# Kernel tuning notes

Hardware: AMD Instinct MI355X
Metric: run time of the kernel (lower is better)

Reference implementation:

```python
import jax, jax.numpy as jnp
import numpy as np

IN_FEATURES = 1024
OUT_FEATURES = 256
BATCH = 131072
EPS = 1e-4


def setup_inputs() -> dict:
    key = jax.random.key(0)
    kx, kw, kb = jax.random.split(key, 3)
    x = jax.random.normal(kx, (BATCH, IN_FEATURES), dtype=jnp.float32)
    # nn.Linear default init: U(-1/sqrt(in), 1/sqrt(in)) for both W and b
    bound = 1.0 / np.sqrt(IN_FEATURES)
    W = jax.random.uniform(kw, (OUT_FEATURES, IN_FEATURES), dtype=jnp.float32, minval=-bound, maxval=bound)
    b = jax.random.uniform(kb, (OUT_FEATURES,), dtype=jnp.float32, minval=-bound, maxval=bound)
    return {"x": x, "W": W, "b": b}


def reference(x, W, b):
    # L2-normalize each row (dim=1), matching x / (||x||_2 + 1e-4)
    norm = jnp.sqrt(jnp.sum(x * x, axis=1, keepdims=True))
    x_dir = x / (norm + EPS)
    # Linear: x_dir @ W^T + b, then ReLU
    h = jnp.einsum('bi,oi->bo', x_dir, W) + b
    return jax.nn.relu(h)
```

## Files before the change

kernel.cpp:

```cpp
#include <hip/hip_runtime.h>


#define IN_F   1024
#define OUT_F  256
#define BATCH  131072
#define BM     128
#define NKT    32
#define EPSV   1e-4f

typedef __attribute__((ext_vector_type(8))) __bf16 bf16x8;
typedef __attribute__((ext_vector_type(4))) __bf16 bf16x4;
typedef __attribute__((ext_vector_type(4))) float  f32x4;

__device__ __forceinline__ void gload_lds16(const void* g, void* lds) {
  __builtin_amdgcn_global_load_lds(
      (const __attribute__((address_space(1))) void*)g,
      (__attribute__((address_space(3))) void*)lds, 16, 0, 0);
}

#define VM_WAIT(N) do { asm volatile("s_waitcnt vmcnt(" #N ")" ::: "memory"); \
                        __builtin_amdgcn_sched_barrier(0); } while (0)

__global__ void wconv_kernel(const float* __restrict__ W, __bf16* __restrict__ Wb) {
  const int t = blockIdx.x * blockDim.x + threadIdx.x;
  const float4 v = reinterpret_cast<const float4*>(W)[t];
  bf16x4 h;
  h[0] = (__bf16)v.x; h[1] = (__bf16)v.y; h[2] = (__bf16)v.z; h[3] = (__bf16)v.w;
  reinterpret_cast<bf16x4*>(Wb)[t] = h;
}

__global__ __launch_bounds__(512, 2)
void ffl_kernel(const float* __restrict__ x, const __bf16* __restrict__ Wb,
                const float* __restrict__ bias, float* __restrict__ out) {
  __shared__ __align__(16) char smem[163840];
  char* const Ab[3] = {smem, smem + 32768, smem + 65536};
  char* const Bb[4] = {smem + 98304, smem + 114688, smem + 131072, smem + 147456};

  const int tid  = threadIdx.x;
  const int lane = tid & 63;
  const int wave = tid >> 6;
  const int wr   = wave >> 2;
  const int wc   = wave & 3;
  const int rm   = lane & 15;
  const int q    = lane >> 4;
  const size_t block_row = (size_t)blockIdx.x * BM;
  const int phg = blockIdx.x & 15;

  const float* aSrc[4]; int aDst[4];
  #pragma unroll
  for (int i = 0; i < 4; ++i) {
    const int c   = 4 * wave + i;
    const int row = 4 * c + (lane >> 4);
    const int s   = (lane & 15) ^ (row & 7);
    aSrc[i] = x + (block_row + row) * IN_F + s * 4;
    aDst[i] = c * 1024;
  }
  const __bf16* bSrc[2]; int bDst[2];
  #pragma unroll
  for (int i = 0; i < 2; ++i) {
    const int c    = 2 * wave + i;
    const int brow = 16 * c + (lane >> 2);
    const int bs   = (lane & 3) ^ ((brow >> 1) & 3);
    bSrc[i] = Wb + (size_t)brow * IN_F + bs * 8;
    bDst[i] = c * 1024;
  }

  f32x4 acc[4][4];
  #pragma unroll
  for (int m = 0; m < 4; ++m)
    #pragma unroll
    for (int n = 0; n < 4; ++n)
      acc[m][n] = (f32x4){0.f, 0.f, 0.f, 0.f};

  float ssq[4] = {0.f, 0.f, 0.f, 0.f};

  auto stageA = [&](int g) {
    const int pg = (g + phg) & 15;
    #pragma unroll
    for (int i = 0; i < 4; ++i)
      gload_lds16(aSrc[i] + pg * 64, Ab[g % 3] + aDst[i]);
  };
  auto stageB = [&](int kt) {
    const int pk = (kt + 2 * phg) & 31;
    #pragma unroll
    for (int i = 0; i < 2; ++i)
      gload_lds16(bSrc[i] + pk * 32, Bb[kt & 3] + bDst[i]);
  };

  stageA(0);
  stageB(0);
  stageA(1);
  stageB(1);
  stageB(2);
  VM_WAIT(8);
  __builtin_amdgcn_s_barrier();

  #pragma unroll
  for (int kt = 0; kt < NKT; ++kt) {
    if (kt + 3 < NKT) stageB(kt + 3);
    if ((kt & 1) == 0 && (kt / 2 + 2) < 16) stageA(kt / 2 + 2);

    const char* abuf = Ab[(kt >> 1) % 3];
    const char* bbuf = Bb[kt & 3];
    const int   gb   = (kt & 1) * 8 + 2 * q;

    bf16x8 aF[4];
    #pragma unroll
    for (int m = 0; m < 4; ++m) {
      const int ra = wr * 64 + m * 16 + rm;
      const char* ab = abuf + ra * 256;
      const int sw = ra & 7;
      const f32x4 lo = *reinterpret_cast<const f32x4*>(ab + ((gb)     ^ sw) * 16);
      const f32x4 hi = *reinterpret_cast<const f32x4*>(ab + ((gb + 1) ^ sw) * 16);
      ssq[m] += lo[0]*lo[0] + lo[1]*lo[1] + lo[2]*lo[2] + lo[3]*lo[3]
              + hi[0]*hi[0] + hi[1]*hi[1] + hi[2]*hi[2] + hi[3]*hi[3];
      bf16x8 a;
      a[0]=(__bf16)lo[0]; a[1]=(__bf16)lo[1]; a[2]=(__bf16)lo[2]; a[3]=(__bf16)lo[3];
      a[4]=(__bf16)hi[0]; a[5]=(__bf16)hi[1]; a[6]=(__bf16)hi[2]; a[7]=(__bf16)hi[3];
      aF[m] = a;
    }

    #pragma unroll
    for (int n = 0; n < 4; ++n) {
      const int rb = wc * 64 + n * 16 + rm;
      const bf16x8 bF = *reinterpret_cast<const bf16x8*>(
          bbuf + rb * 64 + (q ^ ((rb >> 1) & 3)) * 16);
      #pragma unroll
      for (int m = 0; m < 4; ++m)
        acc[m][n] = __builtin_amdgcn_mfma_f32_16x16x32_bf16(aF[m], bF, acc[m][n], 0, 0, 0);
    }

    if (kt >= 30)                        { VM_WAIT(0); }
    else if (kt == 29)                   { VM_WAIT(2); }
    else if ((kt & 1) == 0 && kt >= 2 && kt <= 26) { VM_WAIT(12); }
    else                                 { VM_WAIT(8); }
    __builtin_amdgcn_s_barrier();
  }

  #pragma unroll
  for (int m = 0; m < 4; ++m) {
    ssq[m] += __shfl_xor(ssq[m], 16);
    ssq[m] += __shfl_xor(ssq[m], 32);
  }
  float* norms = reinterpret_cast<float*>(smem + 163328);
  if (wc == 0 && q == 0) {
    #pragma unroll
    for (int m = 0; m < 4; ++m)
      norms[wr * 64 + m * 16 + rm] = 1.0f / (sqrtf(ssq[m]) + EPSV);
  }
  __syncthreads();

  float* stg = reinterpret_cast<float*>(smem);
  const int col0 = wc * 64 + rm;
  #pragma unroll
  for (int n = 0; n < 4; ++n) {
    const float bn = bias[col0 + n * 16];
    #pragma unroll
    for (int m = 0; m < 4; ++m) {
      #pragma unroll
      for (int j = 0; j < 4; ++j) {
        const int lr = wr * 64 + m * 16 + q * 4 + j;
        stg[lr * 260 + col0 + n * 16] = fmaxf(acc[m][n][j] * norms[lr] + bn, 0.f);
      }
    }
  }
  __syncthreads();

  const int r = tid >> 3, p = tid & 7;
  #pragma unroll
  for (int half = 0; half < 2; ++half) {
    const int row = half * 64 + r;
    const float* srow = stg + row * 260;
    float* orow = out + (block_row + row) * OUT_F;
    #pragma unroll
    for (int i = 0; i < 8; ++i) {
      const int f = i * 8 + p;
      const f32x4 v = *reinterpret_cast<const f32x4*>(srow + f * 4);
      *reinterpret_cast<f32x4*>(orow + f * 4) = v;
    }
  }
}

extern "C" void kernel_launch(void* const* d_in, const int* in_sizes, int n_in,
                              void* d_out, int out_size, void* d_ws, size_t ws_size,
                              hipStream_t stream) {
  const float* x = (const float*)d_in[0];
  const float* W = (const float*)d_in[1];
  const float* b = (const float*)d_in[2];
  float* out = (float*)d_out;
  __bf16* Wb = (__bf16*)d_ws;

  wconv_kernel<<<(OUT_F * IN_F / 4) / 256, 256, 0, stream>>>(W, Wb);
  ffl_kernel<<<BATCH / BM, 512, 0, stream>>>(x, Wb, b, out);
}
```

Before: 177.6 us.

## Halve LDS footprint to fit two blocks per CU with finer-grained pipeline

Shrinks the shared-memory tiles from 160KB to 80KB so two 512-thread blocks can be resident per CU. A is now staged per 32-wide k-step with triple buffering, and B is double buffered, with simplified waitcnt logic. The epilogue staging is split into two column halves so the output tile fits in the smaller LDS. The goal is more warps in flight to hide global-memory latency on this bandwidth-bound kernel. The cost is a shallower prefetch depth and extra barriers in the epilogue.

```diff
diff --git a/kernel.cpp b/kernel.cpp
--- a/kernel.cpp
+++ b/kernel.cpp
@@ -32,9 +32,9 @@
 __global__ __launch_bounds__(512, 2)
 void ffl_kernel(const float* __restrict__ x, const __bf16* __restrict__ Wb,
                 const float* __restrict__ bias, float* __restrict__ out) {
-  __shared__ __align__(16) char smem[163840];
-  char* const Ab[3] = {smem, smem + 32768, smem + 65536};
-  char* const Bb[4] = {smem + 98304, smem + 114688, smem + 131072, smem + 147456};
+  __shared__ __align__(16) char smem[81920];
+  char* const Ab[3] = {smem, smem + 16384, smem + 32768};
+  char* const Bb[2] = {smem + 49152, smem + 65536};
 
   const int tid  = threadIdx.x;
   const int lane = tid & 63;
@@ -44,15 +44,15 @@
   const int rm   = lane & 15;
   const int q    = lane >> 4;
   const size_t block_row = (size_t)blockIdx.x * BM;
-  const int phg = blockIdx.x & 15;
+  const int phg = blockIdx.x & 31;
 
-  const float* aSrc[4]; int aDst[4];
+  const float* aSrc[2]; int aDst[2];
   #pragma unroll
-  for (int i = 0; i < 4; ++i) {
-    const int c   = 4 * wave + i;
-    const int row = 4 * c + (lane >> 4);
-    const int s   = (lane & 15) ^ (row & 7);
-    aSrc[i] = x + (block_row + row) * IN_F + s * 4;
+  for (int i = 0; i < 2; ++i) {
+    const int c  = 2 * wave + i;
+    const int rl = lane >> 3;
+    const int s  = (lane & 7) ^ rl;
+    aSrc[i] = x + (block_row + 8 * c + rl) * IN_F + s * 4;
     aDst[i] = c * 1024;
   }
   const __bf16* bSrc[2]; int bDst[2];
@@ -74,44 +74,39 @@
 
   float ssq[4] = {0.f, 0.f, 0.f, 0.f};
 
-  auto stageA = [&](int g) {
-    const int pg = (g + phg) & 15;
-    #pragma unroll
-    for (int i = 0; i < 4; ++i)
-      gload_lds16(aSrc[i] + pg * 64, Ab[g % 3] + aDst[i]);
+  auto stageA = [&](int s) {
+    const int pk = (s + phg) & 31;
+    gload_lds16(aSrc[0] + pk * 32, Ab[s % 3] + aDst[0]);
+    gload_lds16(aSrc[1] + pk * 32, Ab[s % 3] + aDst[1]);
   };
-  auto stageB = [&](int kt) {
-    const int pk = (kt + 2 * phg) & 31;
-    #pragma unroll
-    for (int i = 0; i < 2; ++i)
-      gload_lds16(bSrc[i] + pk * 32, Bb[kt & 3] + bDst[i]);
+  auto stageB = [&](int s) {
+    const int pk = (s + phg) & 31;
+    gload_lds16(bSrc[0] + pk * 32, Bb[s & 1] + bDst[0]);
+    gload_lds16(bSrc[1] + pk * 32, Bb[s & 1] + bDst[1]);
   };
 
   stageA(0);
   stageB(0);
   stageA(1);
-  stageB(1);
-  stageB(2);
-  VM_WAIT(8);
+  VM_WAIT(2);
   __builtin_amdgcn_s_barrier();
 
   #pragma unroll
   for (int kt = 0; kt < NKT; ++kt) {
-    if (kt + 3 < NKT) stageB(kt + 3);
-    if ((kt & 1) == 0 && (kt / 2 + 2) < 16) stageA(kt / 2 + 2);
+    if (kt + 1 < NKT) stageB(kt + 1);
+    if (kt + 2 < NKT) stageA(kt + 2);
 
-    const char* abuf = Ab[(kt >> 1) % 3];
-    const char* bbuf = Bb[kt & 3];
-    const int   gb   = (kt & 1) * 8 + 2 * q;
+    const char* abuf = Ab[kt % 3];
+    const char* bbuf = Bb[kt & 1];
 
     bf16x8 aF[4];
     #pragma unroll
     for (int m = 0; m < 4; ++m) {
       const int ra = wr * 64 + m * 16 + rm;
-      const char* ab = abuf + ra * 256;
+      const char* ab = abuf + ra * 128;
       const int sw = ra & 7;
-      const f32x4 lo = *reinterpret_cast<const f32x4*>(ab + ((gb)     ^ sw) * 16);
-      const f32x4 hi = *reinterpret_cast<const f32x4*>(ab + ((gb + 1) ^ sw) * 16);
+      const f32x4 lo = *reinterpret_cast<const f32x4*>(ab + ((2 * q)     ^ sw) * 16);
+      const f32x4 hi = *reinterpret_cast<const f32x4*>(ab + ((2 * q + 1) ^ sw) * 16);
       ssq[m] += lo[0]*lo[0] + lo[1]*lo[1] + lo[2]*lo[2] + lo[3]*lo[3]
               + hi[0]*hi[0] + hi[1]*hi[1] + hi[2]*hi[2] + hi[3]*hi[3];
       bf16x8 a;
@@ -130,10 +125,7 @@
         acc[m][n] = __builtin_amdgcn_mfma_f32_16x16x32_bf16(aF[m], bF, acc[m][n], 0, 0, 0);
     }
 
-    if (kt >= 30)                        { VM_WAIT(0); }
-    else if (kt == 29)                   { VM_WAIT(2); }
-    else if ((kt & 1) == 0 && kt >= 2 && kt <= 26) { VM_WAIT(12); }
-    else                                 { VM_WAIT(8); }
+    if (kt < 30) { VM_WAIT(2); } else { VM_WAIT(0); }
     __builtin_amdgcn_s_barrier();
   }
 
@@ -142,7 +134,7 @@
     ssq[m] += __shfl_xor(ssq[m], 16);
     ssq[m] += __shfl_xor(ssq[m], 32);
   }
-  float* norms = reinterpret_cast<float*>(smem + 163328);
+  float* norms = reinterpret_cast<float*>(smem + 67584);
   if (wc == 0 && q == 0) {
     #pragma unroll
     for (int m = 0; m < 4; ++m)
@@ -152,32 +144,34 @@
 
   float* stg = reinterpret_cast<float*>(smem);
   const int col0 = wc * 64 + rm;
+  const int r = tid >> 2, p = tid & 3;
   #pragma unroll
-  for (int n = 0; n < 4; ++n) {
-    const float bn = bias[col0 + n * 16];
-    #pragma unroll
-    for (int m = 0; m < 4; ++m) {
+  for (int half = 0; half < 2; ++half) {
+    if ((wc >> 1) == half) {
       #pragma unroll
-      for (int j = 0; j < 4; ++j) {
-        const int lr = wr * 64 + m * 16 + q * 4 + j;
-        stg[lr * 260 + col0 + n * 16] = fmaxf(acc[m][n][j] * norms[lr] + bn, 0.f);
+      for (int n = 0; n < 4; ++n) {
+        const float bn = bias[col0 + n * 16];
+        #pragma unroll
+        for (int m = 0; m < 4; ++m) {
+          #pragma unroll
+          for (int j = 0; j < 4; ++j) {
+            const int lr = wr * 64 + m * 16 + q * 4 + j;
+            stg[lr * 132 + (wc & 1) * 64 + n * 16 + rm] =
+                fmaxf(acc[m][n][j] * norms[lr] + bn, 0.f);
+          }
+        }
       }
     }
-  }
-  __syncthreads();
-
-  const int r = tid >> 3, p = tid & 7;
-  #pragma unroll
-  for (int half = 0; half < 2; ++half) {
-    const int row = half * 64 + r;
-    const float* srow = stg + row * 260;
-    float* orow = out + (block_row + row) * OUT_F;
+    __syncthreads();
+    float* orow = out + (block_row + r) * OUT_F + half * 128;
+    const float* srow = stg + r * 132;
     #pragma unroll
     for (int i = 0; i < 8; ++i) {
-      const int f = i * 8 + p;
+      const int f = i * 4 + p;
       const f32x4 v = *reinterpret_cast<const f32x4*>(srow + f * 4);
       *reinterpret_cast<f32x4*>(orow + f * 4) = v;
     }
+    __syncthreads();
   }
 }
 
```

Result: slower. 186.4 us (+5.0%).
